# Kernel optimization log

Measured on AMD Instinct MI355X. Metric: run time of the kernel, lower is better.

## Reference

```python
import jax, jax.numpy as jnp
import numpy as np

VOCAB, EMB, HID = 50000, 256, 512
N, T = 256, 512


def setup_inputs() -> dict:
    key = jax.random.key(0)
    ks = jax.random.split(key, 9)
    s_ih = 1.0 / np.sqrt(HID)
    return {
        "input1": jax.random.randint(ks[0], (N, T), 0, VOCAB, dtype=jnp.int32),
        "input2": jax.random.randint(ks[1], (N, T), 0, VOCAB, dtype=jnp.int32),
        "emb_table": jax.random.normal(ks[2], (VOCAB, EMB), jnp.float32),
        "W_ih": jax.random.normal(ks[3], (4 * HID, EMB), jnp.float32) * s_ih,
        "W_hh": jax.random.normal(ks[4], (4 * HID, HID), jnp.float32) * s_ih,
        "b_ih": jax.random.normal(ks[5], (4 * HID,), jnp.float32) * s_ih,
        "b_hh": jax.random.normal(ks[6], (4 * HID,), jnp.float32) * s_ih,
        "W_fc": jax.random.normal(ks[7], (2, HID), jnp.float32) * s_ih,
        "b_fc": jax.random.normal(ks[8], (2,), jnp.float32) * s_ih,
    }


def _lstm_last_h(tokens, emb_table, W_ih, W_hh, b):
    # tokens: [N, T] int -> embedded [N, T, E]
    x = emb_table[tokens]
    # precompute input projections for all timesteps: [T, N, 4H]
    xg = jnp.einsum("nte,ge->tng", x, W_ih) + b
    h0 = jnp.zeros((tokens.shape[0], HID), x.dtype)
    c0 = jnp.zeros_like(h0)

    def step(carry, xg_t):
        h, c = carry
        gates = xg_t + h @ W_hh.T  # [N, 4H]
        i, f, g, o = jnp.split(gates, 4, axis=-1)
        i, f, o = jax.nn.sigmoid(i), jax.nn.sigmoid(f), jax.nn.sigmoid(o)
        g = jnp.tanh(g)
        c = f * c + i * g
        h = o * jnp.tanh(c)
        return (h, c), None

    (h, _), _ = jax.lax.scan(step, (h0, c0), xg)
    return h  # [N, HID]


def reference(input1, input2, emb_table, W_ih, W_hh, b_ih, b_hh, W_fc, b_fc):
    b = b_ih + b_hh
    h1 = _lstm_last_h(input1, emb_table, W_ih, W_hh, b)
    h2 = _lstm_last_h(input2, emb_table, W_ih, W_hh, b)
    h = h1 * h2  # combo_unit == 'MULT'
    logits = h @ W_fc.T + b_fc  # [N, 2]
    return jax.nn.softmax(logits, axis=1)
```

## Files before the change

### kernel.cpp

```cpp
#include <hip/hip_runtime.h>
#include <stdint.h>

#define VOCAB  50000
#define EMBD   256
#define HIDD   512
#define G4     2048
#define NBAT   256
#define TSEQ   512

#define O_P2    0ull
#define O_EMBT  204800000ull
#define O_WIH   230400000ull
#define O_WHH   231448576ull
#define O_TOKT  233545728ull
#define O_HBUF  234594304ull
#define WS_NEED 235643136ull
#define O_FLAGS O_EMBT

typedef __bf16 bf16x8 __attribute__((ext_vector_type(8)));
typedef float  f32x4  __attribute__((ext_vector_type(4)));
typedef float  f32x16 __attribute__((ext_vector_type(16)));
typedef unsigned long long u64;

__device__ __forceinline__ unsigned short f2bf(float x) {
  unsigned u = __float_as_uint(x);
  u = (u + 0x7fffu + ((u >> 16) & 1u)) >> 16;
  return (unsigned short)u;
}
__device__ __forceinline__ float b2f(unsigned short b) {
  return __uint_as_float(((unsigned)b) << 16);
}
__device__ __forceinline__ float sigf(float x) {
  float e = __builtin_amdgcn_exp2f(-1.4426950408889634f * x);
  return __builtin_amdgcn_rcpf(1.0f + e);
}
__device__ __forceinline__ float tanhf_(float x) {
  float e = __builtin_amdgcn_exp2f(-2.8853900817779268f * x);
  return 2.0f * __builtin_amdgcn_rcpf(1.0f + e) - 1.0f;
}

__global__ void k_prep(const float* __restrict__ emb, const float* __restrict__ wih,
                       const float* __restrict__ whh, const int* __restrict__ tok1,
                       const int* __restrict__ tok2, unsigned short* __restrict__ embT,
                       unsigned short* __restrict__ wihb, unsigned short* __restrict__ whhb,
                       int* __restrict__ tokT, unsigned* __restrict__ hz)
{
  const int stride = gridDim.x * blockDim.x;
  const int id0 = blockIdx.x * blockDim.x + threadIdx.x;
  for (int i = id0; i < VOCAB * EMBD; i += stride) embT[i] = f2bf(emb[i]);
  for (int i = id0; i < G4 * EMBD; i += stride)    wihb[i] = f2bf(wih[i]);
  for (int i = id0; i < G4 * HIDD; i += stride)    whhb[i] = f2bf(whh[i]);
  for (int i = id0; i < 2 * TSEQ * NBAT; i += stride) {
    int l = i >> 17, t = (i >> 8) & 511, n = i & 255;
    tokT[i] = (l ? tok2 : tok1)[n * TSEQ + t];
  }
  for (int i = id0; i < 262144; i += stride) hz[i] = 0u;
}

__global__ void k_zero(unsigned* __restrict__ flags)
{
  const int i = blockIdx.x * blockDim.x + threadIdx.x;
  if (i < 65536) flags[i] = 0u;
}

__global__ __launch_bounds__(256) void
k_proj(const unsigned short* __restrict__ embT, const unsigned short* __restrict__ wihb,
       const float* __restrict__ bih, const float* __restrict__ bhh,
       unsigned short* __restrict__ P2)
{
  const int l  = threadIdx.x & 63;
  const int w  = threadIdx.x >> 6;
  const int n0 = blockIdx.x * 128 + (w & 1) * 64;
  const int m0 = blockIdx.y * 128 + (w >> 1) * 64;
  const int lq = l >> 4, lc = l & 15;

  f32x4 acc[4][4];
  #pragma unroll
  for (int a = 0; a < 4; ++a)
    #pragma unroll
    for (int b = 0; b < 4; ++b) acc[a][b] = (f32x4){0.f, 0.f, 0.f, 0.f};

  const uint8_t* eb = (const uint8_t*)embT;
  const uint8_t* wb = (const uint8_t*)wihb;
  #pragma unroll
  for (int ks = 0; ks < 8; ++ks) {
    const int koff = ks * 64 + lq * 16;
    bf16x8 a[4], b[4];
    #pragma unroll
    for (int mt = 0; mt < 4; ++mt) {
      int row = m0 + mt * 16 + lc; if (row >= VOCAB) row = VOCAB - 1;
      a[mt] = *(const bf16x8*)(eb + (size_t)row * 512 + koff);
    }
    #pragma unroll
    for (int nt = 0; nt < 4; ++nt) {
      int g = n0 + nt * 16 + lc;
      b[nt] = *(const bf16x8*)(wb + (size_t)g * 512 + koff);
    }
    #pragma unroll
    for (int mt = 0; mt < 4; ++mt)
      #pragma unroll
      for (int nt = 0; nt < 4; ++nt)
        acc[mt][nt] = __builtin_amdgcn_mfma_f32_16x16x32_bf16(a[mt], b[nt], acc[mt][nt], 0, 0, 0);
  }

  #pragma unroll
  for (int mt = 0; mt < 4; ++mt)
    #pragma unroll
    for (int r = 0; r < 4; ++r) {
      const int vrow = m0 + mt * 16 + lq * 4 + r;
      if (vrow < VOCAB) {
        #pragma unroll
        for (int nt = 0; nt < 4; ++nt) {
          const int gcol = n0 + nt * 16 + lc;
          float v = acc[mt][nt][r] + bih[gcol] + bhh[gcol];
          const int colp = ((gcol & 511) << 2) | (gcol >> 9);
          P2[(size_t)vrow * 2048 + colp] = f2bf(v);
        }
      }
    }
}

#define GB 32768

__global__ __launch_bounds__(256, 1) void
k_lstm(const uint8_t* __restrict__ P2, const int* __restrict__ tokT,
       const uint8_t* __restrict__ whh, uint8_t* __restrict__ hbuf,
       unsigned* __restrict__ flags)
{
  __shared__ __align__(16) uint8_t smem[163840];
  const int tid  = threadIdx.x;
  const int l    = tid & 63;
  const int w    = tid >> 6;
  const int bid  = blockIdx.x;
  const int jb   = bid & 15;
  const int mg   = (bid >> 4) & 7;
  const int lstm = bid >> 7;
  const int grp  = bid >> 4;
  const int m0   = mg * 32;
  const int j0   = jb * 32;

  const size_t hslot = (size_t)NBAT * HIDD * 2;
  const int em   = tid >> 3;
  const int ecol = tid & 7;
  const int an   = l & 31;
  const int ah   = l >> 5;

  bf16x8 wreg[32];
  {
    const uint8_t* wrow = whh + (size_t)(w * 512 + j0 + an) * 1024 + (size_t)ah * 16;
    #pragma unroll
    for (int ks = 0; ks < 32; ++ks)
      wreg[ks] = *(const bf16x8*)(wrow + ks * 32);
  }

  const unsigned* fpoll = flags + (size_t)(grp * 64 + l) * 64;
  unsigned* fmine = flags + (size_t)(grp * 64 + jb * 4 + w) * 64;

  float cst[4] = {0.f, 0.f, 0.f, 0.f};
  int tok_next = tokT[(lstm * TSEQ + 0) * NBAT + m0 + em];

  for (int t = 0; t < TSEQ; ++t) {
    const int tok_cur = tok_next;

    const uint8_t* xsrc = P2 + (size_t)tok_cur * 4096 + (size_t)j0 * 8 + (size_t)ecol * 32;
    const uint4 xq0 = *(const uint4*)(xsrc);
    const uint4 xq1 = *(const uint4*)(xsrc + 16);
    if (t + 1 < TSEQ) tok_next = tokT[(lstm * TSEQ + (t + 1)) * NBAT + m0 + em];

    if (t > 0) {
      const unsigned tgt = (unsigned)t;
      int guard = 0;
      for (;;) {
        const unsigned v = __hip_atomic_load(fpoll, __ATOMIC_RELAXED, __HIP_MEMORY_SCOPE_AGENT);
        if (__all((int)(v >= tgt))) break;
        __builtin_amdgcn_s_sleep(1);
        if (++guard > 400000) break;
      }
    }

    {
      const uint8_t* hb = hbuf + (size_t)(lstm * 2 + (t & 1)) * hslot
                        + (size_t)m0 * 1024 + (size_t)tid * 8;
      u64 v[16];
      #pragma unroll
      for (int i = 0; i < 16; ++i)
        v[i] = __hip_atomic_load((const u64*)(hb + (size_t)i * 2048),
                                 __ATOMIC_RELAXED, __HIP_MEMORY_SCOPE_AGENT);
      #pragma unroll
      for (int i = 0; i < 16; ++i) {
        const int m = i * 2 + (tid >> 7);
        const int c = (tid >> 1) & 63;
        const int half = tid & 1;
        *(u64*)(smem + (size_t)m * 1024 + ((c ^ (m & 7)) * 16) + half * 8) = v[i];
      }
    }
    __syncthreads();

    f32x16 acc0{}, acc1{};
    #pragma unroll
    for (int ks = 0; ks < 32; ++ks) {
      const int ch = ks * 2 + ah;
      const bf16x8 av = *(const bf16x8*)(smem + (size_t)an * 1024 + ((ch ^ (an & 7)) * 16));
      if (ks & 1) acc1 = __builtin_amdgcn_mfma_f32_32x32x16_bf16(av, wreg[ks], acc1, 0, 0, 0);
      else        acc0 = __builtin_amdgcn_mfma_f32_32x32x16_bf16(av, wreg[ks], acc0, 0, 0, 0);
    }

    {
      float* gb = (float*)(smem + GB);
      #pragma unroll
      for (int r = 0; r < 16; ++r) {
        const int row = (r & 3) + 8 * (r >> 2) + 4 * ah;
        gb[w * 1024 + row * 32 + an] = acc0[r] + acc1[r];
      }
    }
    __syncthreads();

    {
      const float* gb = (const float*)(smem + GB);
      const f32x4 pi = *(const f32x4*)(gb + 0 * 1024 + em * 32 + ecol * 4);
      const f32x4 pf = *(const f32x4*)(gb + 1 * 1024 + em * 32 + ecol * 4);
      const f32x4 pg = *(const f32x4*)(gb + 2 * 1024 + em * 32 + ecol * 4);
      const f32x4 po = *(const f32x4*)(gb + 3 * 1024 + em * 32 + ecol * 4);
      unsigned short xsv[16];
      *(uint4*)(xsv) = xq0;
      *(uint4*)(xsv + 8) = xq1;
      unsigned short hv[4];
      #pragma unroll
      for (int k = 0; k < 4; ++k) {
        const float iv = sigf(pi[k] + b2f(xsv[k * 4 + 0]));
        const float fv = sigf(pf[k] + b2f(xsv[k * 4 + 1]));
        const float gv = tanhf_(pg[k] + b2f(xsv[k * 4 + 2]));
        const float ov = sigf(po[k] + b2f(xsv[k * 4 + 3]));
        const float cv = fv * cst[k] + iv * gv;
        cst[k] = cv;
        hv[k] = f2bf(ov * tanhf_(cv));
      }
      const u64 hp = (u64)hv[0] | ((u64)hv[1] << 16) | ((u64)hv[2] << 32) | ((u64)hv[3] << 48);
      uint8_t* hdst = hbuf + (size_t)(lstm * 2 + ((t + 1) & 1)) * hslot
                    + (size_t)(m0 + em) * 1024 + (size_t)(j0 + ecol * 4) * 2;
      __hip_atomic_store((u64*)hdst, hp, __ATOMIC_RELAXED, __HIP_MEMORY_SCOPE_AGENT);
    }
    asm volatile("s_waitcnt vmcnt(0)" ::: "memory");
    if (l == 0 && t + 1 < TSEQ)
      __hip_atomic_store(fmine, (unsigned)(t + 1),
                         __ATOMIC_RELAXED, __HIP_MEMORY_SCOPE_AGENT);
  }
}

__global__ __launch_bounds__(64) void
k_fc(const uint8_t* __restrict__ hbuf, const float* __restrict__ wfc,
     const float* __restrict__ bfc, float* __restrict__ out)
{
  const int n = blockIdx.x, l = threadIdx.x;
  const unsigned short* h1 = (const unsigned short*)(hbuf) + (size_t)n * HIDD;
  const unsigned short* h2 = (const unsigned short*)(hbuf + 2 * (size_t)NBAT * HIDD * 2) + (size_t)n * HIDD;
  float s0 = 0.f, s1 = 0.f;
  for (int j = l; j < HIDD; j += 64) {
    float hv = b2f(h1[j]) * b2f(h2[j]);
    s0 += hv * wfc[j];
    s1 += hv * wfc[HIDD + j];
  }
  #pragma unroll
  for (int off = 32; off > 0; off >>= 1) {
    s0 += __shfl_down(s0, off, 64);
    s1 += __shfl_down(s1, off, 64);
  }
  if (l == 0) {
    s0 += bfc[0]; s1 += bfc[1];
    float m  = fmaxf(s0, s1);
    float e0 = __builtin_amdgcn_exp2f((s0 - m) * 1.4426950408889634f);
    float e1 = __builtin_amdgcn_exp2f((s1 - m) * 1.4426950408889634f);
    float inv = 1.0f / (e0 + e1);
    out[n * 2 + 0] = e0 * inv;
    out[n * 2 + 1] = e1 * inv;
  }
}

extern "C" void kernel_launch(void* const* d_in, const int* in_sizes, int n_in,
                              void* d_out, int out_size, void* d_ws, size_t ws_size,
                              hipStream_t stream) {
  (void)in_sizes; (void)n_in; (void)out_size;
  if (ws_size < WS_NEED) return;

  const int*   tok1 = (const int*)d_in[0];
  const int*   tok2 = (const int*)d_in[1];
  const float* emb  = (const float*)d_in[2];
  const float* wih  = (const float*)d_in[3];
  const float* whh  = (const float*)d_in[4];
  const float* bih  = (const float*)d_in[5];
  const float* bhh  = (const float*)d_in[6];
  const float* wfc  = (const float*)d_in[7];
  const float* bfc  = (const float*)d_in[8];
  float* out = (float*)d_out;

  uint8_t* ws = (uint8_t*)d_ws;
  unsigned short* P2    = (unsigned short*)(ws + O_P2);
  unsigned short* embT  = (unsigned short*)(ws + O_EMBT);
  unsigned short* wihb  = (unsigned short*)(ws + O_WIH);
  unsigned short* whhb  = (unsigned short*)(ws + O_WHH);
  int*            tokT  = (int*)(ws + O_TOKT);
  uint8_t*        hbuf  = ws + O_HBUF;
  unsigned*       flags = (unsigned*)(ws + O_FLAGS);

  k_prep<<<1024, 256, 0, stream>>>(emb, wih, whh, tok1, tok2, embT, wihb, whhb,
                                   tokT, (unsigned*)hbuf);
  k_proj<<<dim3(16, 391), 256, 0, stream>>>(embT, wihb, bih, bhh, P2);
  k_zero<<<256, 256, 0, stream>>>(flags);

  {
    const uint8_t* p2p = (const uint8_t*)P2;
    const int*     tkp = tokT;
    const uint8_t* whp = (const uint8_t*)whhb;
    uint8_t*       hbp = hbuf;
    unsigned*      flp = flags;
    void* args[5] = {(void*)&p2p, (void*)&tkp, (void*)&whp, (void*)&hbp, (void*)&flp};
    hipError_t e = hipLaunchCooperativeKernel((void*)k_lstm, dim3(256), dim3(256),
                                              args, 0, stream);
    if (e != hipSuccess) {
      (void)hipGetLastError();
      k_lstm<<<256, 256, 0, stream>>>(p2p, tkp, whp, hbp, flp);
    }
  }

  k_fc<<<256, 64, 0, stream>>>(hbuf, wfc, bfc, out);
}
```

Before: 2.185 ms.

## Aggregate per-wave flags into one per-block flag and widen h-state loads

Each block now publishes a single progress flag, raised by whichever wave is last to finish (counted with an LDS atomic), instead of four per-wave flags. Only wave 0 polls 16 flags per group and then releases the block with a barrier, which cuts the global flag traffic and polling work on the recurrent critical path. The hidden-state gather now uses 16-byte loads with cache-bypass bits through inline assembly, replacing 8-byte atomic loads. This adds an extra __syncthreads per step and relies on the sc0/sc1 bits for coherence across blocks.

```diff
diff --git a/kernel.cpp b/kernel.cpp
--- a/kernel.cpp
+++ b/kernel.cpp
@@ -60,7 +60,7 @@
 __global__ void k_zero(unsigned* __restrict__ flags)
 {
   const int i = blockIdx.x * blockDim.x + threadIdx.x;
-  if (i < 65536) flags[i] = 0u;
+  if (i < 16384) flags[i] = 0u;
 }
 
 __global__ __launch_bounds__(256) void
@@ -120,7 +120,8 @@
     }
 }
 
-#define GB 32768
+#define GB  32768
+#define CNT 49152
 
 __global__ __launch_bounds__(256, 1) void
 k_lstm(const uint8_t* __restrict__ P2, const int* __restrict__ tokT,
@@ -145,6 +146,8 @@
   const int an   = l & 31;
   const int ah   = l >> 5;
 
+  if (tid == 0) *(volatile unsigned*)(smem + CNT) = 0u;
+
   bf16x8 wreg[32];
   {
     const uint8_t* wrow = whh + (size_t)(w * 512 + j0 + an) * 1024 + (size_t)ah * 16;
@@ -153,8 +156,8 @@
       wreg[ks] = *(const bf16x8*)(wrow + ks * 32);
   }
 
-  const unsigned* fpoll = flags + (size_t)(grp * 64 + l) * 64;
-  unsigned* fmine = flags + (size_t)(grp * 64 + jb * 4 + w) * 64;
+  const unsigned* fpoll = flags + (size_t)(grp * 16 + (l & 15)) * 64;
+  unsigned* fmine = flags + (size_t)bid * 64;
 
   float cst[4] = {0.f, 0.f, 0.f, 0.f};
   int tok_next = tokT[(lstm * TSEQ + 0) * NBAT + m0 + em];
@@ -167,7 +170,7 @@
     const uint4 xq1 = *(const uint4*)(xsrc + 16);
     if (t + 1 < TSEQ) tok_next = tokT[(lstm * TSEQ + (t + 1)) * NBAT + m0 + em];
 
-    if (t > 0) {
+    if (t > 0 && w == 0) {
       const unsigned tgt = (unsigned)t;
       int guard = 0;
       for (;;) {
@@ -177,21 +180,24 @@
         if (++guard > 400000) break;
       }
     }
+    __syncthreads();
 
     {
       const uint8_t* hb = hbuf + (size_t)(lstm * 2 + (t & 1)) * hslot
-                        + (size_t)m0 * 1024 + (size_t)tid * 8;
-      u64 v[16];
-      #pragma unroll
-      for (int i = 0; i < 16; ++i)
-        v[i] = __hip_atomic_load((const u64*)(hb + (size_t)i * 2048),
-                                 __ATOMIC_RELAXED, __HIP_MEMORY_SCOPE_AGENT);
-      #pragma unroll
-      for (int i = 0; i < 16; ++i) {
-        const int m = i * 2 + (tid >> 7);
-        const int c = (tid >> 1) & 63;
-        const int half = tid & 1;
-        *(u64*)(smem + (size_t)m * 1024 + ((c ^ (m & 7)) * 16) + half * 8) = v[i];
+                        + (size_t)m0 * 1024
+                        + (size_t)(tid >> 7) * 2048 + (size_t)(tid & 127) * 16;
+      uint4 v[8];
+      #pragma unroll
+      for (int i = 0; i < 8; ++i)
+        asm volatile("global_load_dwordx4 %0, %1, off sc0 sc1"
+                     : "=v"(v[i]) : "v"(hb + (size_t)i * 4096));
+      asm volatile("s_waitcnt vmcnt(0)" ::: "memory");
+      __builtin_amdgcn_sched_barrier(0);
+      const int c16 = tid & 63;
+      #pragma unroll
+      for (int i = 0; i < 8; ++i) {
+        const int m = i * 4 + 2 * (tid >> 7) + ((tid >> 6) & 1);
+        *(uint4*)(smem + (size_t)m * 1024 + ((c16 ^ (m & 7)) * 16)) = v[i];
       }
     }
     __syncthreads();
@@ -240,10 +246,14 @@
                     + (size_t)(m0 + em) * 1024 + (size_t)(j0 + ecol * 4) * 2;
       __hip_atomic_store((u64*)hdst, hp, __ATOMIC_RELAXED, __HIP_MEMORY_SCOPE_AGENT);
     }
+
     asm volatile("s_waitcnt vmcnt(0)" ::: "memory");
-    if (l == 0 && t + 1 < TSEQ)
-      __hip_atomic_store(fmine, (unsigned)(t + 1),
-                         __ATOMIC_RELAXED, __HIP_MEMORY_SCOPE_AGENT);
+    if (l == 0 && t + 1 < TSEQ) {
+      const unsigned old = atomicAdd((unsigned*)(smem + CNT), 1u);
+      if (old == (unsigned)(4 * t + 3))
+        __hip_atomic_store(fmine, (unsigned)(t + 1),
+                           __ATOMIC_RELAXED, __HIP_MEMORY_SCOPE_AGENT);
+    }
   }
 }
 
@@ -305,7 +315,7 @@
   k_prep<<<1024, 256, 0, stream>>>(emb, wih, whh, tok1, tok2, embT, wihb, whhb,
                                    tokT, (unsigned*)hbuf);
   k_proj<<<dim3(16, 391), 256, 0, stream>>>(embT, wihb, bih, bhh, P2);
-  k_zero<<<256, 256, 0, stream>>>(flags);
+  k_zero<<<64, 256, 0, stream>>>(flags);
 
   {
     const uint8_t* p2p = (const uint8_t*)P2;
```

Result: no change. 2.176 ms (-0.4%).
